# Kernel optimization log

Hardware: AMD Instinct MI355X
Metric: run time of the kernel (lower is better)

Reference implementation:

```python
import itertools
import jax, jax.numpy as jnp
import numpy as np


def setup_inputs() -> dict:
    key = jax.random.key(0)
    k1, k2 = jax.random.split(key)
    B, N, D = 32, 32, 16          # batch, n_objects, rel_dim
    F, K = 16, 3                  # n_filters, kernel_size
    R = jax.random.normal(k1, (B, N, N, D), dtype=jnp.float32)
    filters = jax.random.normal(k2, (F, K, K, D), dtype=jnp.float32)
    return {"R": R, "filters": filters}


def reference(R, filters):
    # R: (B, n_objects, n_objects, rel_dim); filters: (n_filters, k, k, rel_dim)
    B, n_objects, _, rel_dim = R.shape
    k = filters.shape[1]
    # groups_type='combinations': all size-k index combinations (static, shape (G, k))
    groups = jnp.asarray(
        list(itertools.combinations(range(n_objects), k)), dtype=jnp.int32
    )
    # Vectorized per-group double gather: (B, G, k, k, rel_dim)
    R_sub = R[:, groups[:, :, None], groups[:, None, :], :]
    # Relational inner product against all filters: sum over (i, j, d)
    # -> (B, n_groups, n_filters)
    return jnp.einsum("bgijd,fijd->bgf", R_sub, filters)
```

## Files before the change

### kernel.cpp

```cpp
#include <hip/hip_runtime.h>
#include <stdint.h>


#define NOBJ 32
#define NG   4960
#define NF   16
#define ND   16
#define KPAD 168
#define GPB  64

typedef __bf16 bf16x8 __attribute__((ext_vector_type(8)));
typedef float  f32x4  __attribute__((ext_vector_type(4)));

__device__ __forceinline__ unsigned f2bf1(float x) {
    unsigned u = __float_as_uint(x);
    return (u + 0x7fffu + ((u >> 16) & 1u)) >> 16;
}
__device__ __forceinline__ unsigned packbf(float lo, float hi) {
    return f2bf1(lo) | (f2bf1(hi) << 16);
}

__device__ __forceinline__ void unrank3(int g, int& t0, int& t1, int& t2) {
    int rem = g;
    t0 = 0;
    for (;;) { int c = ((31 - t0) * (30 - t0)) >> 1; if (rem < c) break; rem -= c; ++t0; }
    t1 = t0 + 1;
    for (;;) { int c = 31 - t1; if (rem < c) break; rem -= c; ++t1; }
    t2 = t1 + 1 + rem;
}

__global__ __launch_bounds__(256) void rgc_mfma(
    const float* __restrict__ R,
    const float* __restrict__ Fw,
    float* __restrict__ out)
{
    __shared__ unsigned short sbuf[(GPB + NF) * KPAD];
    unsigned short* sA = sbuf;
    unsigned short* sW = sbuf + GPB * KPAD;

    const int tid = threadIdx.x;
    const int b   = blockIdx.y;
    const int g0  = blockIdx.x * GPB;

    for (int idx = tid; idx < (GPB + NF) * 6; idx += 256) {
        const int row = idx / 6, q = idx - row * 6;
        *(uint2*)&sbuf[row * KPAD + 144 + q * 4] = make_uint2(0u, 0u);
    }

    for (int e = tid; e < NF * 144; e += 256) {
        const int f = e / 144, k = e - f * 144;
        sW[f * KPAD + k] = (unsigned short)f2bf1(Fw[e]);
    }

    {
        const int gi = tid >> 2, q = tid & 3;
        const int g  = min(g0 + gi, NG - 1);
        int t0, t1, t2;
        unrank3(g, t0, t1, t2);
        const int t[3] = {t0, t1, t2};
        const float* Rb = R + (size_t)b * (NOBJ * NOBJ * ND);
#pragma unroll
        for (int ij = 0; ij < 9; ++ij) {
            const int i = ij / 3, j = ij - i * 3;
            const float4 v = *(const float4*)(Rb + (t[i] * NOBJ + t[j]) * ND + q * 4);
            uint2 pk;
            pk.x = packbf(v.x, v.y);
            pk.y = packbf(v.z, v.w);
            *(uint2*)&sA[gi * KPAD + ij * ND + q * 4] = pk;
        }
    }

    __syncthreads();

    const int wave = tid >> 6;
    const int lane = tid & 63;
    const int l15  = lane & 15;
    const int quad = lane >> 4;

    const unsigned short* aRow = sA + (wave * 16 + l15) * KPAD + quad * 8;
    const unsigned short* bRow = sW + l15 * KPAD + quad * 8;

    f32x4 acc = {0.f, 0.f, 0.f, 0.f};
#pragma unroll
    for (int s = 0; s < 5; ++s) {
        const bf16x8 af = *(const bf16x8*)(aRow + s * 32);
        const bf16x8 bf = *(const bf16x8*)(bRow + s * 32);
        acc = __builtin_amdgcn_mfma_f32_16x16x32_bf16(af, bf, acc, 0, 0, 0);
    }

    const int gbase = g0 + wave * 16 + quad * 4;
#pragma unroll
    for (int r = 0; r < 4; ++r) {
        const int g = gbase + r;
        if (g < NG) out[((size_t)b * NG + g) * NF + l15] = acc[r];
    }
}

extern "C" void kernel_launch(void* const* d_in, const int* in_sizes, int n_in,
                              void* d_out, int out_size, void* d_ws, size_t ws_size,
                              hipStream_t stream) {
    const float* R  = (const float*)d_in[0];
    const float* Fw = (const float*)d_in[1];
    if (n_in >= 2 && in_sizes[0] == NF * 9 * ND) { R = (const float*)d_in[1]; Fw = (const float*)d_in[0]; }
    float* out = (float*)d_out;
    dim3 grid((NG + GPB - 1) / GPB, 32);
    rgc_mfma<<<grid, dim3(256, 1, 1), 0, stream>>>(R, Fw, out);
}
```

Baseline: 68.18 us.

## Precast R and filters to bf16 in a prepass and gather MFMA operands directly

Adds a prepass kernel that converts R to bf16 and pads the filter matrix into workspace. The main kernel then drops shared memory and __syncthreads and loads the MFMA A operands straight from the bf16 copy of R in global memory, with each lane computing its own row offsets. The goal is to stop redoing the fp32-to-bf16 conversion and LDS staging in every block and to halve the bytes gathered. In exchange it adds a second kernel launch and a round trip of R through workspace memory.

Result: faster. 66.81 us (-2.0%).

```diff
diff --git a/kernel.cpp b/kernel.cpp
--- a/kernel.cpp
+++ b/kernel.cpp
@@ -6,8 +6,8 @@
 #define NG   4960
 #define NF   16
 #define ND   16
-#define KPAD 168
-#define GPB  64
+#define KP   160
+#define RELEMS (32 * NOBJ * NOBJ * ND)
 
 typedef __bf16 bf16x8 __attribute__((ext_vector_type(8)));
 typedef float  f32x4  __attribute__((ext_vector_type(4)));
@@ -29,70 +29,84 @@
     t2 = t1 + 1 + rem;
 }
 
-__global__ __launch_bounds__(256) void rgc_mfma(
-    const float* __restrict__ R,
-    const float* __restrict__ Fw,
+__global__ __launch_bounds__(256) void rgc_pre(
+    const float* __restrict__ R, const float* __restrict__ Fw,
+    unsigned short* __restrict__ Rbf, unsigned short* __restrict__ Wpad)
+{
+    const int tid = threadIdx.x;
+    if (blockIdx.x < 256) {
+        const int e = (blockIdx.x * 256 + tid) * 8;
+        const float4* p = (const float4*)(R + e);
+        const float4 v0 = p[0], v1 = p[1];
+        uint4 o;
+        o.x = packbf(v0.x, v0.y); o.y = packbf(v0.z, v0.w);
+        o.z = packbf(v1.x, v1.y); o.w = packbf(v1.z, v1.w);
+        *(uint4*)(Rbf + e) = o;
+    } else {
+        for (int e = tid * 8; e < NF * KP; e += 256 * 8) {
+            const int f = e / KP, k0 = e % KP;
+            uint4 o = make_uint4(0u, 0u, 0u, 0u);
+            if (k0 < 144) {
+                const float4* p = (const float4*)(Fw + f * 144 + k0);
+                const float4 v0 = p[0], v1 = p[1];
+                o.x = packbf(v0.x, v0.y); o.y = packbf(v0.z, v0.w);
+                o.z = packbf(v1.x, v1.y); o.w = packbf(v1.z, v1.w);
+            }
+            *(uint4*)(Wpad + e) = o;
+        }
+    }
+}
+
+__global__ __launch_bounds__(256) void rgc_main(
+    const unsigned short* __restrict__ Rbf,
+    const unsigned short* __restrict__ Wpad,
     float* __restrict__ out)
 {
-    __shared__ unsigned short sbuf[(GPB + NF) * KPAD];
-    unsigned short* sA = sbuf;
-    unsigned short* sW = sbuf + GPB * KPAD;
-
-    const int tid = threadIdx.x;
-    const int b   = blockIdx.y;
-    const int g0  = blockIdx.x * GPB;
-
-    for (int idx = tid; idx < (GPB + NF) * 6; idx += 256) {
-        const int row = idx / 6, q = idx - row * 6;
-        *(uint2*)&sbuf[row * KPAD + 144 + q * 4] = make_uint2(0u, 0u);
-    }
-
-    for (int e = tid; e < NF * 144; e += 256) {
-        const int f = e / 144, k = e - f * 144;
-        sW[f * KPAD + k] = (unsigned short)f2bf1(Fw[e]);
-    }
-
-    {
-        const int gi = tid >> 2, q = tid & 3;
-        const int g  = min(g0 + gi, NG - 1);
-        int t0, t1, t2;
-        unrank3(g, t0, t1, t2);
-        const int t[3] = {t0, t1, t2};
-        const float* Rb = R + (size_t)b * (NOBJ * NOBJ * ND);
-#pragma unroll
-        for (int ij = 0; ij < 9; ++ij) {
-            const int i = ij / 3, j = ij - i * 3;
-            const float4 v = *(const float4*)(Rb + (t[i] * NOBJ + t[j]) * ND + q * 4);
-            uint2 pk;
-            pk.x = packbf(v.x, v.y);
-            pk.y = packbf(v.z, v.w);
-            *(uint2*)&sA[gi * KPAD + ij * ND + q * 4] = pk;
-        }
-    }
-
-    __syncthreads();
-
+    const int tid  = threadIdx.x;
     const int wave = tid >> 6;
     const int lane = tid & 63;
     const int l15  = lane & 15;
     const int quad = lane >> 4;
+    const int b    = blockIdx.y;
+    const int gw   = blockIdx.x * 64 + wave * 16;
 
-    const unsigned short* aRow = sA + (wave * 16 + l15) * KPAD + quad * 8;
-    const unsigned short* bRow = sW + l15 * KPAD + quad * 8;
+    const int g = min(gw + l15, NG - 1);
+    int t0, t1, t2;
+    unrank3(g, t0, t1, t2);
+    const int t[3] = {t0, t1, t2};
+
+    int rowoff[9];
+#pragma unroll
+    for (int ij = 0; ij < 9; ++ij) {
+        const int i = ij / 3, j = ij % 3;
+        rowoff[ij] = (t[i] * NOBJ + t[j]) * ND;
+    }
+
+    const int hi = quad >> 1;
+    const int d0 = (quad & 1) * 8;
+    int ro[5];
+    ro[0] = hi ? rowoff[1] : rowoff[0];
+    ro[1] = hi ? rowoff[3] : rowoff[2];
+    ro[2] = hi ? rowoff[5] : rowoff[4];
+    ro[3] = hi ? rowoff[7] : rowoff[6];
+    ro[4] = rowoff[8];
+
+    const unsigned short* Rb    = Rbf + (size_t)b * (NOBJ * NOBJ * ND);
+    const unsigned short* wbase = Wpad + l15 * KP + quad * 8;
 
     f32x4 acc = {0.f, 0.f, 0.f, 0.f};
 #pragma unroll
     for (int s = 0; s < 5; ++s) {
-        const bf16x8 af = *(const bf16x8*)(aRow + s * 32);
-        const bf16x8 bf = *(const bf16x8*)(bRow + s * 32);
-        acc = __builtin_amdgcn_mfma_f32_16x16x32_bf16(af, bf, acc, 0, 0, 0);
+        const bf16x8 a = *(const bf16x8*)(Rb + ro[s] + d0);
+        const bf16x8 w = *(const bf16x8*)(wbase + s * 32);
+        acc = __builtin_amdgcn_mfma_f32_16x16x32_bf16(a, w, acc, 0, 0, 0);
     }
 
-    const int gbase = g0 + wave * 16 + quad * 4;
+    const int gbase = gw + quad * 4;
 #pragma unroll
     for (int r = 0; r < 4; ++r) {
-        const int g = gbase + r;
-        if (g < NG) out[((size_t)b * NG + g) * NF + l15] = acc[r];
+        const int gg = gbase + r;
+        if (gg < NG) out[((size_t)b * NG + gg) * NF + l15] = acc[r];
     }
 }
 
@@ -103,6 +117,11 @@
     const float* Fw = (const float*)d_in[1];
     if (n_in >= 2 && in_sizes[0] == NF * 9 * ND) { R = (const float*)d_in[1]; Fw = (const float*)d_in[0]; }
     float* out = (float*)d_out;
-    dim3 grid((NG + GPB - 1) / GPB, 32);
-    rgc_mfma<<<grid, dim3(256, 1, 1), 0, stream>>>(R, Fw, out);
+
+    unsigned short* Rbf  = (unsigned short*)d_ws;
+    unsigned short* Wpad = (unsigned short*)((char*)d_ws + RELEMS * 2);
+
+    rgc_pre<<<dim3(257, 1), dim3(256, 1, 1), 0, stream>>>(R, Fw, Rbf, Wpad);
+    dim3 grid((NG + 63) / 64, 32);
+    rgc_main<<<grid, dim3(256, 1, 1), 0, stream>>>(Rbf, Wpad, out);
 }
```
